# Kernel tuning notes

Measured on AMD Instinct MI355X. Metric: run time of the kernel, lower is better.

## Reference

```python
import jax, jax.numpy as jnp
import numpy as np

ALPHA = 0.1   # alpha_factor
BETA = 1.0    # beta_factor
NUM_CLASSES = 1000
B, D = 4096, 512


def setup_inputs() -> dict:
    key = jax.random.key(0)
    ks = jax.random.split(key, 7)
    return {
        "anchor": jax.random.normal(ks[0], (B, D), dtype=jnp.float32),
        "positive": jax.random.normal(ks[1], (B, D), dtype=jnp.float32),
        "negative": jax.random.normal(ks[2], (B, D), dtype=jnp.float32),
        "outputs": jax.random.normal(ks[3], (3 * B, NUM_CLASSES), dtype=jnp.float32),
        "labels_anchor": jax.random.randint(ks[4], (B,), 0, NUM_CLASSES, dtype=jnp.int32).astype(jnp.int64),
        "labels_neg": jax.random.randint(ks[5], (B,), 0, NUM_CLASSES, dtype=jnp.int32).astype(jnp.int64),
        "exemplars": jax.random.normal(ks[6], (NUM_CLASSES, D), dtype=jnp.float32),
    }


def reference(anchor, positive, negative, outputs, labels_anchor, labels_neg, exemplars):
    # cross-entropy (mean reduction) over concatenated labels [3B]
    labels = jnp.concatenate([labels_anchor, labels_anchor, labels_neg], axis=0)
    logp = jax.nn.log_softmax(outputs, axis=-1)                       # [3B, C]
    loss_softmax = -jnp.mean(jnp.take_along_axis(logp, labels[:, None], axis=1))

    # pairwise L2 distances anchor-to-exemplars via ||a||^2 + ||e||^2 - 2 a.e  -> [B, C]
    a_sq = jnp.sum(anchor * anchor, axis=1, keepdims=True)            # [B, 1]
    e_sq = jnp.sum(exemplars * exemplars, axis=1)[None, :]            # [1, C]
    d2 = a_sq + e_sq - 2.0 * (anchor @ exemplars.T)                   # [B, C]
    d_all = jnp.sqrt(jnp.maximum(d2, 0.0))

    d_ref = jnp.take_along_axis(d_all, labels_anchor[:, None], axis=1)[:, 0]  # [B]
    d_closest = jnp.min(d_all, axis=1)                                # [B]
    loss_center = jnp.sum(jax.nn.relu(d_ref - d_closest))

    tp = jnp.linalg.norm(anchor - positive, axis=1)                   # [B]
    tn = jnp.linalg.norm(anchor - negative, axis=1)                   # [B]
    loss_triplet = jnp.sum(jax.nn.relu(tp - tn))

    loss_total = loss_softmax + ALPHA * loss_center + BETA * loss_triplet
    return (loss_total, loss_triplet, loss_softmax, loss_center)
```

## Files before the change

### kernel.cpp

```cpp
#include <hip/hip_runtime.h>
#include <math.h>

#define BB 4096
#define DD 512
#define CC 1000

typedef __attribute__((ext_vector_type(8))) short short8;
typedef __attribute__((ext_vector_type(4))) float f32x4;

#define OFF_ABF  0
#define OFF_EBF  1048576
#define OFF_ESQ  1310720
#define OFF_ASQ  1311744
#define OFF_DREF 1315840
#define OFF_PMIN 1319936
#define OFF_CEP  1324032
#define OFF_TRP  1327104

__device__ __forceinline__ unsigned short f2bf(float x) {
    unsigned u = __float_as_uint(x);
    unsigned r = (u + 0x7FFFu + ((u >> 16) & 1u)) >> 16;
    return (unsigned short)r;
}

__global__ __launch_bounds__(512) void prep_kernel(
    const float* __restrict__ a, const float* __restrict__ p,
    const float* __restrict__ n, const float* __restrict__ ex,
    const int* __restrict__ la,
    unsigned short* __restrict__ Abf, unsigned short* __restrict__ Ebf,
    float* __restrict__ esq, float* __restrict__ asq,
    float* __restrict__ dref, float* __restrict__ tr_part,
    float* __restrict__ pmin)
{
    __shared__ float ps[8];
    const int bid = blockIdx.x;
    const int tid = threadIdx.x;
    const int w = tid >> 6, lane = tid & 63;

    if (bid < 512) {
        const int i = bid * 8 + w;
        const int label = la[i];
        const float4* ar = (const float4*)(a + (size_t)i * DD);
        const float4* pr = (const float4*)(p + (size_t)i * DD);
        const float4* nr = (const float4*)(n + (size_t)i * DD);
        const float4* er = (const float4*)(ex + (size_t)label * DD);
        float sa = 0.f, sp = 0.f, sn = 0.f, se = 0.f;
#pragma unroll
        for (int k = 0; k < 2; k++) {
            const int j = lane + k * 64;
            float4 av = ar[j], pv = pr[j], nv = nr[j], ev = er[j];
            union { unsigned short u[4]; uint2 q; } o;
            o.u[0]=f2bf(av.x); o.u[1]=f2bf(av.y); o.u[2]=f2bf(av.z); o.u[3]=f2bf(av.w);
            *(uint2*)(Abf + (size_t)i * DD + j * 4) = o.q;
            sa += av.x*av.x + av.y*av.y + av.z*av.z + av.w*av.w;
            float dx = av.x-pv.x, dy = av.y-pv.y, dz = av.z-pv.z, dw = av.w-pv.w;
            sp += dx*dx + dy*dy + dz*dz + dw*dw;
            dx = av.x-nv.x; dy = av.y-nv.y; dz = av.z-nv.z; dw = av.w-nv.w;
            sn += dx*dx + dy*dy + dz*dz + dw*dw;
            dx = av.x-ev.x; dy = av.y-ev.y; dz = av.z-ev.z; dw = av.w-ev.w;
            se += dx*dx + dy*dy + dz*dz + dw*dw;
        }
        for (int off = 32; off; off >>= 1) {
            sa += __shfl_xor(sa, off);
            sp += __shfl_xor(sp, off);
            sn += __shfl_xor(sn, off);
            se += __shfl_xor(se, off);
        }
        if (lane == 0) {
            asq[i]  = sa;
            dref[i] = sqrtf(se);
            pmin[i] = INFINITY;
            ps[w] = fmaxf(sqrtf(sp) - sqrtf(sn), 0.f);
        }
        __syncthreads();
        if (tid == 0) {
            float t = 0.f;
#pragma unroll
            for (int q = 0; q < 8; q++) t += ps[q];
            tr_part[bid] = t;
        }
    } else {
        const int c = (bid - 512) * 8 + w;
        float s = 0.f;
        if (c < CC) {
            const float4* row = (const float4*)(ex + (size_t)c * DD);
#pragma unroll
            for (int k = 0; k < 2; k++) {
                const int j = lane + k * 64;
                float4 v = row[j];
                union { unsigned short u[4]; uint2 q; } o;
                o.u[0]=f2bf(v.x); o.u[1]=f2bf(v.y); o.u[2]=f2bf(v.z); o.u[3]=f2bf(v.w);
                *(uint2*)(Ebf + (size_t)c * DD + j * 4) = o.q;
                s += v.x*v.x + v.y*v.y + v.z*v.z + v.w*v.w;
            }
            for (int off = 32; off; off >>= 1) s += __shfl_xor(s, off);
        } else {
            const uint2 z = make_uint2(0, 0);
#pragma unroll
            for (int k = 0; k < 2; k++) {
                const int j = lane + k * 64;
                *(uint2*)(Ebf + (size_t)c * DD + j * 4) = z;
            }
        }
        if (lane == 0) esq[c] = s;
    }
}

#define GL2LDS(gsrc, ldst) __builtin_amdgcn_global_load_lds( \
    (const __attribute__((address_space(1))) unsigned int*)(gsrc), \
    (__attribute__((address_space(3))) unsigned int*)(ldst), 16, 0, 0)

__global__ __launch_bounds__(512) void main_kernel(
    const unsigned short* __restrict__ Ab, const unsigned short* __restrict__ Eb,
    const float* __restrict__ asq, const float* __restrict__ esq,
    const float* __restrict__ outp,
    const int* __restrict__ la, const int* __restrict__ ln,
    float* __restrict__ pmin, float* __restrict__ ce_part)
{
    __shared__ unsigned short lA[128 * 64];
    __shared__ unsigned short lB[128 * 64];
    __shared__ float s_pm[4][128];
    __shared__ float ps[8];

    const int bid = blockIdx.x;
    const int tid = threadIdx.x;
    const int w = tid >> 6, lane = tid & 63;

    if (bid < 256) {
        const int strip = bid & 31, panel = bid >> 5;
        const int gm0 = strip * 128, gn0 = panel * 128;
        const int wm = w >> 2, wn = w & 3;
        const int hi = lane >> 4, lo = lane & 15;

        size_t srcA[2], srcB[2]; int dst2[2];
#pragma unroll
        for (int i = 0; i < 2; i++) {
            int c = tid + i * 512, r = c >> 3, s = c & 7;
            srcA[i] = ((size_t)(gm0 + r) << 9) + ((s ^ (r & 7)) << 3);
            srcB[i] = ((size_t)(gn0 + r) << 9) + ((s ^ (r & 7)) << 3);
            dst2[i] = c << 3;
        }

        f32x4 acc[4][2];
#pragma unroll
        for (int mi = 0; mi < 4; mi++)
#pragma unroll
            for (int ni = 0; ni < 2; ni++) acc[mi][ni] = (f32x4){0.f, 0.f, 0.f, 0.f};

        for (int kt = 0; kt < 8; kt++) {
#pragma unroll
            for (int i = 0; i < 2; i++) {
                GL2LDS(Ab + srcA[i] + (kt << 6), &lA[dst2[i]]);
                GL2LDS(Eb + srcB[i] + (kt << 6), &lB[dst2[i]]);
            }
            asm volatile("s_waitcnt vmcnt(0)" ::: "memory");
            __builtin_amdgcn_s_barrier();
            asm volatile("" ::: "memory");

#pragma unroll
            for (int kk = 0; kk < 2; kk++) {
                short8 af[4], bf[2];
#pragma unroll
                for (int mi = 0; mi < 4; mi++) {
                    int r = (wm << 6) + (mi << 4) + lo, s = (kk << 2) + hi;
                    af[mi] = *(const short8*)&lA[(r << 6) + ((s ^ (r & 7)) << 3)];
                }
#pragma unroll
                for (int ni = 0; ni < 2; ni++) {
                    int r = (wn << 5) + (ni << 4) + lo, s = (kk << 2) + hi;
                    bf[ni] = *(const short8*)&lB[(r << 6) + ((s ^ (r & 7)) << 3)];
                }
#pragma unroll
                for (int mi = 0; mi < 4; mi++)
#pragma unroll
                    for (int ni = 0; ni < 2; ni++)
                        acc[mi][ni] = __builtin_amdgcn_mfma_f32_16x16x32_bf16(af[mi], bf[ni], acc[mi][ni], 0, 0, 0);
            }
            asm volatile("" ::: "memory");
            __builtin_amdgcn_s_barrier();
        }

        float aq[4][4];
#pragma unroll
        for (int mi = 0; mi < 4; mi++) {
            float4 a0 = *(const float4*)&asq[gm0 + wm * 64 + mi * 16 + hi * 4];
            aq[mi][0]=a0.x; aq[mi][1]=a0.y; aq[mi][2]=a0.z; aq[mi][3]=a0.w;
        }
        float esqc[2]; int bad[2];
#pragma unroll
        for (int ni = 0; ni < 2; ni++) {
            int gn = gn0 + wn * 32 + ni * 16 + lo;
            esqc[ni] = esq[gn];
            bad[ni] = (gn >= CC);
        }
        float vmin[4][4];
#pragma unroll
        for (int mi = 0; mi < 4; mi++)
#pragma unroll
            for (int j = 0; j < 4; j++) {
                float best = INFINITY;
#pragma unroll
                for (int ni = 0; ni < 2; ni++) {
                    float d2 = aq[mi][j] + esqc[ni] - 2.f * acc[mi][ni][j];
                    float d = sqrtf(fmaxf(d2, 0.f));
                    if (bad[ni]) d = INFINITY;
                    best = fminf(best, d);
                }
                vmin[mi][j] = best;
            }
#pragma unroll
        for (int off = 1; off < 16; off <<= 1)
#pragma unroll
            for (int mi = 0; mi < 4; mi++)
#pragma unroll
                for (int j = 0; j < 4; j++)
                    vmin[mi][j] = fminf(vmin[mi][j], __shfl_xor(vmin[mi][j], off));

        if (lo == 0) {
#pragma unroll
            for (int mi = 0; mi < 4; mi++)
#pragma unroll
                for (int j = 0; j < 4; j++)
                    s_pm[wn][wm * 64 + mi * 16 + hi * 4 + j] = vmin[mi][j];
        }
        __syncthreads();
        if (tid < 128) {
            float m2 = fminf(fminf(s_pm[0][tid], s_pm[1][tid]),
                             fminf(s_pm[2][tid], s_pm[3][tid]));
            atomicMin((int*)pmin + gm0 + tid, __float_as_int(m2));
        }
    } else {
        const int cb = bid - 256;
        const int r = cb * 8 + w;
        const int label = (r < 2 * BB) ? la[r & (BB - 1)] : ln[r - 2 * BB];
        const float4* row4 = (const float4*)(outp + (size_t)r * CC);
        float4 v[4];
#pragma unroll
        for (int k = 0; k < 4; k++) {
            int j4 = lane + k * 64;
            v[k] = (j4 < 250) ? row4[j4]
                              : make_float4(-INFINITY, -INFINITY, -INFINITY, -INFINITY);
        }
        float m = -INFINITY;
#pragma unroll
        for (int k = 0; k < 4; k++)
            m = fmaxf(m, fmaxf(fmaxf(v[k].x, v[k].y), fmaxf(v[k].z, v[k].w)));
        for (int off = 32; off; off >>= 1) m = fmaxf(m, __shfl_xor(m, off));

        const int lj4 = label >> 2, lc = label & 3;
        float s = 0.f, lv = 0.f;
#pragma unroll
        for (int k = 0; k < 4; k++) {
            int j4 = lane + k * 64;
            s += __expf(v[k].x - m) + __expf(v[k].y - m)
               + __expf(v[k].z - m) + __expf(v[k].w - m);
            float comp = (lc == 0) ? v[k].x : (lc == 1) ? v[k].y : (lc == 2) ? v[k].z : v[k].w;
            lv += (j4 == lj4) ? comp : 0.f;
        }
        for (int off = 32; off; off >>= 1) {
            s += __shfl_xor(s, off);
            lv += __shfl_xor(lv, off);
        }
        if (lane == 0) ps[w] = -(lv - m - __logf(s));
        __syncthreads();
        if (tid == 0) {
            float t = 0.f;
#pragma unroll
            for (int q = 0; q < 8; q++) t += ps[q];
            ce_part[cb] = t;
        }
    }
}

__global__ __launch_bounds__(1024) void final_kernel(
    const float* __restrict__ ce_part, const float* __restrict__ tr_part,
    const float* __restrict__ pmin, const float* __restrict__ dref,
    float* __restrict__ out)
{
    int tid = threadIdx.x;
    float ce = 0.f, tr = (tid < 512) ? tr_part[tid] : 0.f, ctr = 0.f;
    if (tid < 1536) ce = ce_part[tid] + ((tid < 512) ? ce_part[tid + 1024] : 0.f);
#pragma unroll
    for (int a = 0; a < 4; a++) {
        int m = a * 1024 + tid;
        ctr += fmaxf(dref[m] - pmin[m], 0.f);
    }
    for (int off = 32; off; off >>= 1) {
        ce += __shfl_xor(ce, off);
        tr += __shfl_xor(tr, off);
        ctr += __shfl_xor(ctr, off);
    }
    __shared__ float s[3][16];
    int wid = tid >> 6, lane = tid & 63;
    if (lane == 0) { s[0][wid] = ce; s[1][wid] = tr; s[2][wid] = ctr; }
    __syncthreads();
    if (tid == 0) {
        float tce = 0.f, ttr = 0.f, tctr = 0.f;
#pragma unroll
        for (int w = 0; w < 16; w++) { tce += s[0][w]; ttr += s[1][w]; tctr += s[2][w]; }
        float lsm = tce / (3.f * BB);
        out[0] = lsm + 0.1f * tctr + 1.0f * ttr;
        out[1] = ttr;
        out[2] = lsm;
        out[3] = tctr;
    }
}

extern "C" void kernel_launch(void* const* d_in, const int* in_sizes, int n_in,
                              void* d_out, int out_size, void* d_ws, size_t ws_size,
                              hipStream_t stream) {
    const float* anchor   = (const float*)d_in[0];
    const float* positive = (const float*)d_in[1];
    const float* negative = (const float*)d_in[2];
    const float* outputs  = (const float*)d_in[3];
    const int*   la       = (const int*)d_in[4];
    const int*   ln       = (const int*)d_in[5];
    const float* ex       = (const float*)d_in[6];
    float* out = (float*)d_out;
    float* ws  = (float*)d_ws;

    unsigned short* Abf = (unsigned short*)(ws + OFF_ABF);
    unsigned short* Ebf = (unsigned short*)(ws + OFF_EBF);
    float* esq      = ws + OFF_ESQ;
    float* asq      = ws + OFF_ASQ;
    float* dref     = ws + OFF_DREF;
    float* pmin     = ws + OFF_PMIN;
    float* ce_part  = ws + OFF_CEP;
    float* tr_part  = ws + OFF_TRP;

    hipLaunchKernelGGL(prep_kernel,  dim3(640),  dim3(512),  0, stream,
                       anchor, positive, negative, ex, la, Abf, Ebf, esq, asq, dref, tr_part, pmin);
    hipLaunchKernelGGL(main_kernel,  dim3(1792), dim3(512),  0, stream,
                       Abf, Ebf, asq, esq, outputs, la, ln, pmin, ce_part);
    hipLaunchKernelGGL(final_kernel, dim3(1),    dim3(1024), 0, stream,
                       ce_part, tr_part, pmin, dref, out);
}
```

Measured before the change: 31.40 us.

## Fuse bf16 conversion into GEMM tile loads and drop the prep kernel

Removes the separate prep kernel. The GEMM blocks now load fp32 anchor and exemplar tiles directly, convert them to bf16 in registers, and store them to LDS. Row squared norms are accumulated during that conversion, and the next tile's global loads are issued before the MFMA loop to overlap with compute. Triplet/dref work moves to extra blocks of the same launch, and per-panel minima are written to a partials array instead of atomicMin, so pmin no longer needs initialising. This saves a launch and the bf16 workspace round trip, but replaces async global-to-LDS loads with register staging and redoes the conversion in every panel that reuses the same rows.

Result: slower. 33.52 us (+6.7%).

```diff
diff --git a/kernel.cpp b/kernel.cpp
--- a/kernel.cpp
+++ b/kernel.cpp
@@ -8,14 +8,10 @@
 typedef __attribute__((ext_vector_type(8))) short short8;
 typedef __attribute__((ext_vector_type(4))) float f32x4;
 
-#define OFF_ABF  0
-#define OFF_EBF  1048576
-#define OFF_ESQ  1310720
-#define OFF_ASQ  1311744
-#define OFF_DREF 1315840
-#define OFF_PMIN 1319936
-#define OFF_CEP  1324032
-#define OFF_TRP  1327104
+#define OFF_PMINP 0
+#define OFF_DREF  32768
+#define OFF_CEP   36864
+#define OFF_TRP   38400
 
 __device__ __forceinline__ unsigned short f2bf(float x) {
     unsigned u = __float_as_uint(x);
@@ -23,103 +19,27 @@
     return (unsigned short)r;
 }
 
-__global__ __launch_bounds__(512) void prep_kernel(
+__device__ __forceinline__ short8 cvt8(const float4 x, const float4 y, float& sq) {
+    union { unsigned short u[8]; short8 v; } o;
+    o.u[0]=f2bf(x.x); o.u[1]=f2bf(x.y); o.u[2]=f2bf(x.z); o.u[3]=f2bf(x.w);
+    o.u[4]=f2bf(y.x); o.u[5]=f2bf(y.y); o.u[6]=f2bf(y.z); o.u[7]=f2bf(y.w);
+    sq += x.x*x.x + x.y*x.y + x.z*x.z + x.w*x.w
+        + y.x*y.x + y.y*y.y + y.z*y.z + y.w*y.w;
+    return o.v;
+}
+
+__global__ __launch_bounds__(512) void main_kernel(
     const float* __restrict__ a, const float* __restrict__ p,
     const float* __restrict__ n, const float* __restrict__ ex,
-    const int* __restrict__ la,
-    unsigned short* __restrict__ Abf, unsigned short* __restrict__ Ebf,
-    float* __restrict__ esq, float* __restrict__ asq,
-    float* __restrict__ dref, float* __restrict__ tr_part,
-    float* __restrict__ pmin)
-{
-    __shared__ float ps[8];
-    const int bid = blockIdx.x;
-    const int tid = threadIdx.x;
-    const int w = tid >> 6, lane = tid & 63;
-
-    if (bid < 512) {
-        const int i = bid * 8 + w;
-        const int label = la[i];
-        const float4* ar = (const float4*)(a + (size_t)i * DD);
-        const float4* pr = (const float4*)(p + (size_t)i * DD);
-        const float4* nr = (const float4*)(n + (size_t)i * DD);
-        const float4* er = (const float4*)(ex + (size_t)label * DD);
-        float sa = 0.f, sp = 0.f, sn = 0.f, se = 0.f;
-#pragma unroll
-        for (int k = 0; k < 2; k++) {
-            const int j = lane + k * 64;
-            float4 av = ar[j], pv = pr[j], nv = nr[j], ev = er[j];
-            union { unsigned short u[4]; uint2 q; } o;
-            o.u[0]=f2bf(av.x); o.u[1]=f2bf(av.y); o.u[2]=f2bf(av.z); o.u[3]=f2bf(av.w);
-            *(uint2*)(Abf + (size_t)i * DD + j * 4) = o.q;
-            sa += av.x*av.x + av.y*av.y + av.z*av.z + av.w*av.w;
-            float dx = av.x-pv.x, dy = av.y-pv.y, dz = av.z-pv.z, dw = av.w-pv.w;
-            sp += dx*dx + dy*dy + dz*dz + dw*dw;
-            dx = av.x-nv.x; dy = av.y-nv.y; dz = av.z-nv.z; dw = av.w-nv.w;
-            sn += dx*dx + dy*dy + dz*dz + dw*dw;
-            dx = av.x-ev.x; dy = av.y-ev.y; dz = av.z-ev.z; dw = av.w-ev.w;
-            se += dx*dx + dy*dy + dz*dz + dw*dw;
-        }
-        for (int off = 32; off; off >>= 1) {
-            sa += __shfl_xor(sa, off);
-            sp += __shfl_xor(sp, off);
-            sn += __shfl_xor(sn, off);
-            se += __shfl_xor(se, off);
-        }
-        if (lane == 0) {
-            asq[i]  = sa;
-            dref[i] = sqrtf(se);
-            pmin[i] = INFINITY;
-            ps[w] = fmaxf(sqrtf(sp) - sqrtf(sn), 0.f);
-        }
-        __syncthreads();
-        if (tid == 0) {
-            float t = 0.f;
-#pragma unroll
-            for (int q = 0; q < 8; q++) t += ps[q];
-            tr_part[bid] = t;
-        }
-    } else {
-        const int c = (bid - 512) * 8 + w;
-        float s = 0.f;
-        if (c < CC) {
-            const float4* row = (const float4*)(ex + (size_t)c * DD);
-#pragma unroll
-            for (int k = 0; k < 2; k++) {
-                const int j = lane + k * 64;
-                float4 v = row[j];
-                union { unsigned short u[4]; uint2 q; } o;
-                o.u[0]=f2bf(v.x); o.u[1]=f2bf(v.y); o.u[2]=f2bf(v.z); o.u[3]=f2bf(v.w);
-                *(uint2*)(Ebf + (size_t)c * DD + j * 4) = o.q;
-                s += v.x*v.x + v.y*v.y + v.z*v.z + v.w*v.w;
-            }
-            for (int off = 32; off; off >>= 1) s += __shfl_xor(s, off);
-        } else {
-            const uint2 z = make_uint2(0, 0);
-#pragma unroll
-            for (int k = 0; k < 2; k++) {
-                const int j = lane + k * 64;
-                *(uint2*)(Ebf + (size_t)c * DD + j * 4) = z;
-            }
-        }
-        if (lane == 0) esq[c] = s;
-    }
-}
-
-#define GL2LDS(gsrc, ldst) __builtin_amdgcn_global_load_lds( \
-    (const __attribute__((address_space(1))) unsigned int*)(gsrc), \
-    (__attribute__((address_space(3))) unsigned int*)(ldst), 16, 0, 0)
-
-__global__ __launch_bounds__(512) void main_kernel(
-    const unsigned short* __restrict__ Ab, const unsigned short* __restrict__ Eb,
-    const float* __restrict__ asq, const float* __restrict__ esq,
     const float* __restrict__ outp,
     const int* __restrict__ la, const int* __restrict__ ln,
-    float* __restrict__ pmin, float* __restrict__ ce_part)
+    float* __restrict__ pminp, float* __restrict__ ce_part,
+    float* __restrict__ tr_part, float* __restrict__ dref)
 {
     __shared__ unsigned short lA[128 * 64];
     __shared__ unsigned short lB[128 * 64];
     __shared__ float s_pm[4][128];
+    __shared__ float s_aq[128], s_eq[128];
     __shared__ float ps[8];
 
     const int bid = blockIdx.x;
@@ -132,30 +52,38 @@
         const int wm = w >> 2, wn = w & 3;
         const int hi = lane >> 4, lo = lane & 15;
 
-        size_t srcA[2], srcB[2]; int dst2[2];
-#pragma unroll
-        for (int i = 0; i < 2; i++) {
-            int c = tid + i * 512, r = c >> 3, s = c & 7;
-            srcA[i] = ((size_t)(gm0 + r) << 9) + ((s ^ (r & 7)) << 3);
-            srcB[i] = ((size_t)(gn0 + r) << 9) + ((s ^ (r & 7)) << 3);
-            dst2[i] = c << 3;
-        }
-
+        const int r0 = tid >> 3, s0 = tid & 7;
+        const int g0 = s0 ^ (r0 & 7);
+        const float4* srcA0 = (const float4*)(a + (size_t)(gm0 + r0) * DD) + (g0 << 1);
+        const float4* srcA1 = (const float4*)(a + (size_t)(gm0 + 64 + r0) * DD) + (g0 << 1);
+        const int er0 = gn0 + r0,      er0c = er0 < CC ? er0 : CC - 1;
+        const int er1 = gn0 + 64 + r0, er1c = er1 < CC ? er1 : CC - 1;
+        const float4* srcB0 = (const float4*)(ex + (size_t)er0c * DD) + (g0 << 1);
+        const float4* srcB1 = (const float4*)(ex + (size_t)er1c * DD) + (g0 << 1);
+
+        float4 a0, a0b, a1, a1b, b0, b0b, b1, b1b;
+#define GLOAD(kt) do { \
+        a0 = srcA0[(kt)*16]; a0b = srcA0[(kt)*16 + 1]; \
+        a1 = srcA1[(kt)*16]; a1b = srcA1[(kt)*16 + 1]; \
+        b0 = srcB0[(kt)*16]; b0b = srcB0[(kt)*16 + 1]; \
+        b1 = srcB1[(kt)*16]; b1b = srcB1[(kt)*16 + 1]; \
+    } while (0)
+
+        float sa0 = 0.f, sa1 = 0.f, se0 = 0.f, se1 = 0.f;
         f32x4 acc[4][2];
 #pragma unroll
         for (int mi = 0; mi < 4; mi++)
 #pragma unroll
             for (int ni = 0; ni < 2; ni++) acc[mi][ni] = (f32x4){0.f, 0.f, 0.f, 0.f};
 
+        GLOAD(0);
         for (int kt = 0; kt < 8; kt++) {
-#pragma unroll
-            for (int i = 0; i < 2; i++) {
-                GL2LDS(Ab + srcA[i] + (kt << 6), &lA[dst2[i]]);
-                GL2LDS(Eb + srcB[i] + (kt << 6), &lB[dst2[i]]);
-            }
-            asm volatile("s_waitcnt vmcnt(0)" ::: "memory");
-            __builtin_amdgcn_s_barrier();
-            asm volatile("" ::: "memory");
+            *(short8*)&lA[tid << 3]         = cvt8(a0, a0b, sa0);
+            *(short8*)&lA[(tid + 512) << 3] = cvt8(a1, a1b, sa1);
+            *(short8*)&lB[tid << 3]         = cvt8(b0, b0b, se0);
+            *(short8*)&lB[(tid + 512) << 3] = cvt8(b1, b1b, se1);
+            __syncthreads();
+            if (kt < 7) GLOAD(kt + 1);
 
 #pragma unroll
             for (int kk = 0; kk < 2; kk++) {
@@ -176,21 +104,34 @@
                     for (int ni = 0; ni < 2; ni++)
                         acc[mi][ni] = __builtin_amdgcn_mfma_f32_16x16x32_bf16(af[mi], bf[ni], acc[mi][ni], 0, 0, 0);
             }
-            asm volatile("" ::: "memory");
-            __builtin_amdgcn_s_barrier();
-        }
+            __syncthreads();
+        }
+#undef GLOAD
+
+#pragma unroll
+        for (int off = 1; off < 8; off <<= 1) {
+            sa0 += __shfl_xor(sa0, off);
+            sa1 += __shfl_xor(sa1, off);
+            se0 += __shfl_xor(se0, off);
+            se1 += __shfl_xor(se1, off);
+        }
+        if ((lane & 7) == 0) {
+            s_aq[r0] = sa0; s_aq[64 + r0] = sa1;
+            s_eq[r0] = se0; s_eq[64 + r0] = se1;
+        }
+        __syncthreads();
 
         float aq[4][4];
 #pragma unroll
-        for (int mi = 0; mi < 4; mi++) {
-            float4 a0 = *(const float4*)&asq[gm0 + wm * 64 + mi * 16 + hi * 4];
-            aq[mi][0]=a0.x; aq[mi][1]=a0.y; aq[mi][2]=a0.z; aq[mi][3]=a0.w;
-        }
+        for (int mi = 0; mi < 4; mi++)
+#pragma unroll
+            for (int j = 0; j < 4; j++)
+                aq[mi][j] = s_aq[wm * 64 + mi * 16 + hi * 4 + j];
         float esqc[2]; int bad[2];
 #pragma unroll
         for (int ni = 0; ni < 2; ni++) {
             int gn = gn0 + wn * 32 + ni * 16 + lo;
-            esqc[ni] = esq[gn];
+            esqc[ni] = s_eq[wn * 32 + ni * 16 + lo];
             bad[ni] = (gn >= CC);
         }
         float vmin[4][4];
@@ -227,9 +168,9 @@
         if (tid < 128) {
             float m2 = fminf(fminf(s_pm[0][tid], s_pm[1][tid]),
                              fminf(s_pm[2][tid], s_pm[3][tid]));
-            atomicMin((int*)pmin + gm0 + tid, __float_as_int(m2));
-        }
-    } else {
+            pminp[((size_t)(gm0 + tid) << 3) + panel] = m2;
+        }
+    } else if (bid < 1792) {
         const int cb = bid - 256;
         const int r = cb * 8 + w;
         const int label = (r < 2 * BB) ? la[r & (BB - 1)] : ln[r - 2 * BB];
@@ -269,21 +210,63 @@
             for (int q = 0; q < 8; q++) t += ps[q];
             ce_part[cb] = t;
         }
+    } else {
+        const int i = (bid - 1792) * 8 + w;
+        const int label = la[i];
+        const float4* ar = (const float4*)(a + (size_t)i * DD);
+        const float4* pr = (const float4*)(p + (size_t)i * DD);
+        const float4* nr = (const float4*)(n + (size_t)i * DD);
+        const float4* er = (const float4*)(ex + (size_t)label * DD);
+        float sp = 0.f, sn = 0.f, se = 0.f;
+#pragma unroll
+        for (int k = 0; k < 2; k++) {
+            const int j = lane + k * 64;
+            float4 av = ar[j], pv = pr[j], nv = nr[j], ev = er[j];
+            float dx = av.x-pv.x, dy = av.y-pv.y, dz = av.z-pv.z, dw = av.w-pv.w;
+            sp += dx*dx + dy*dy + dz*dz + dw*dw;
+            dx = av.x-nv.x; dy = av.y-nv.y; dz = av.z-nv.z; dw = av.w-nv.w;
+            sn += dx*dx + dy*dy + dz*dz + dw*dw;
+            dx = av.x-ev.x; dy = av.y-ev.y; dz = av.z-ev.z; dw = av.w-ev.w;
+            se += dx*dx + dy*dy + dz*dz + dw*dw;
+        }
+        for (int off = 32; off; off >>= 1) {
+            sp += __shfl_xor(sp, off);
+            sn += __shfl_xor(sn, off);
+            se += __shfl_xor(se, off);
+        }
+        if (lane == 0) {
+            dref[i] = sqrtf(se);
+            ps[w] = fmaxf(sqrtf(sp) - sqrtf(sn), 0.f);
+        }
+        __syncthreads();
+        if (tid == 0) {
+            float t = 0.f;
+#pragma unroll
+            for (int q = 0; q < 8; q++) t += ps[q];
+            tr_part[bid - 1792] = t;
+        }
     }
 }
 
 __global__ __launch_bounds__(1024) void final_kernel(
     const float* __restrict__ ce_part, const float* __restrict__ tr_part,
-    const float* __restrict__ pmin, const float* __restrict__ dref,
+    const float* __restrict__ pminp, const float* __restrict__ dref,
     float* __restrict__ out)
 {
     int tid = threadIdx.x;
-    float ce = 0.f, tr = (tid < 512) ? tr_part[tid] : 0.f, ctr = 0.f;
-    if (tid < 1536) ce = ce_part[tid] + ((tid < 512) ? ce_part[tid + 1024] : 0.f);
-#pragma unroll
-    for (int a = 0; a < 4; a++) {
-        int m = a * 1024 + tid;
-        ctr += fmaxf(dref[m] - pmin[m], 0.f);
+    float ce = ce_part[tid] + ((tid < 512) ? ce_part[tid + 1024] : 0.f);
+    float tr = (tid < 512) ? tr_part[tid] : 0.f;
+    float ctr = 0.f;
+    float4 d4 = *(const float4*)&dref[tid * 4];
+#pragma unroll
+    for (int k = 0; k < 4; k++) {
+        int m = tid * 4 + k;
+        float4 p0 = *(const float4*)&pminp[(size_t)m * 8];
+        float4 p1 = *(const float4*)&pminp[(size_t)m * 8 + 4];
+        float mn = fminf(fminf(fminf(p0.x, p0.y), fminf(p0.z, p0.w)),
+                         fminf(fminf(p1.x, p1.y), fminf(p1.z, p1.w)));
+        float dr = (k == 0) ? d4.x : (k == 1) ? d4.y : (k == 2) ? d4.z : d4.w;
+        ctr += fmaxf(dr - mn, 0.f);
     }
     for (int off = 32; off; off >>= 1) {
         ce += __shfl_xor(ce, off);
@@ -297,7 +280,7 @@
     if (tid == 0) {
         float tce = 0.f, ttr = 0.f, tctr = 0.f;
 #pragma unroll
-        for (int w = 0; w < 16; w++) { tce += s[0][w]; ttr += s[1][w]; tctr += s[2][w]; }
+        for (int q = 0; q < 16; q++) { tce += s[0][q]; ttr += s[1][q]; tctr += s[2][q]; }
         float lsm = tce / (3.f * BB);
         out[0] = lsm + 0.1f * tctr + 1.0f * ttr;
         out[1] = ttr;
@@ -319,19 +302,14 @@
     float* out = (float*)d_out;
     float* ws  = (float*)d_ws;
 
-    unsigned short* Abf = (unsigned short*)(ws + OFF_ABF);
-    unsigned short* Ebf = (unsigned short*)(ws + OFF_EBF);
-    float* esq      = ws + OFF_ESQ;
-    float* asq      = ws + OFF_ASQ;
+    float* pminp    = ws + OFF_PMINP;
     float* dref     = ws + OFF_DREF;
-    float* pmin     = ws + OFF_PMIN;
     float* ce_part  = ws + OFF_CEP;
     float* tr_part  = ws + OFF_TRP;
 
-    hipLaunchKernelGGL(prep_kernel,  dim3(640),  dim3(512),  0, stream,
-                       anchor, positive, negative, ex, la, Abf, Ebf, esq, asq, dref, tr_part, pmin);
-    hipLaunchKernelGGL(main_kernel,  dim3(1792), dim3(512),  0, stream,
-                       Abf, Ebf, asq, esq, outputs, la, ln, pmin, ce_part);
+    hipLaunchKernelGGL(main_kernel,  dim3(2304), dim3(512),  0, stream,
+                       anchor, positive, negative, ex, outputs, la, ln,
+                       pminp, ce_part, tr_part, dref);
     hipLaunchKernelGGL(final_kernel, dim3(1),    dim3(1024), 0, stream,
-                       ce_part, tr_part, pmin, dref, out);
-}
+                       ce_part, tr_part, pminp, dref, out);
+}
```
